# Optimization experiments

Measured on AMD Instinct MI355X. Metric: run time of the kernel, lower is better.

## Reference

```python
import jax, jax.numpy as jnp
from jax import lax
import numpy as np

GAMMA = 0.1
BIG = 1e8  # finite stand-in for +inf so grads/logsumexp stay clean

# solar radius in km; HUX propagates from 21.5 Rs (WSA inner boundary) to 1 AU (215 Rs)
RS_KM = 6.957e5
R0 = 21.5 * RS_KM
R1 = 215.0 * RS_KM
NR = 200  # radial steps (CFL ~ 0.5 for v~300 km/s, T=512)


def _hux(v_in, omega):
    """HUX-f upwind radial propagation. v_in: [B,T] km/s, omega: [B] rad/s."""
    B, T = v_in.shape
    dr = (R1 - R0) / NR
    dphi = 2.0 * jnp.pi / T  # one Carrington rotation over T samples
    om = omega[:, None]

    def step(v, _):
        dv = jnp.roll(v, -1, axis=1) - v  # periodic longitude
        v_new = v + (dr * om / (jnp.maximum(v, 1.0) * dphi)) * dv
        return v_new, None

    v_out, _ = lax.scan(step, v_in, None, length=NR)
    return v_out


def _soft_dtw(x, y, gamma):
    """Soft-DTW (Cuturi & Blondel). x,y: [B,T,1]. Returns [B]."""
    B, T, _ = x.shape
    # pairwise squared-euclidean cost  [B,T,T]
    D = jnp.sum((x[:, :, None, :] - y[:, None, :, :]) ** 2, axis=-1)
    i = jnp.arange(T)

    def softmin(a, b, c):
        return -gamma * jax.nn.logsumexp(-jnp.stack([a, b, c], 0) / gamma, axis=0)

    # anti-diagonal wavefront: r1[i] = R[i, p-1-i], r2[i] = R[i, p-2-i]
    def step(carry, p):
        r2, r1 = carry
        j = p - i
        valid = (j >= 0) & (j < T)
        d = D[:, i, jnp.clip(j, 0, T - 1)]          # [B,T] cost on diag p
        n_up = jnp.concatenate([jnp.full((B, 1), BIG, D.dtype), r1[:, :-1]], 1)   # R[i-1, p-i]
        n_left = r1                                                                # R[i, p-i-1]
        n_diag = jnp.concatenate([jnp.full((B, 1), BIG, D.dtype), r2[:, :-1]], 1)  # R[i-1, p-i-1]
        r_new = d + softmin(n_up, n_left, n_diag)
        r_new = jnp.where(valid[None, :], r_new, BIG)
        return (r1, r_new), None

    r0 = jnp.full((B, T), BIG, D.dtype).at[:, 0].set(D[:, 0, 0])  # diag p=0: R[0,0]=D[0,0]
    rm1 = jnp.full((B, T), BIG, D.dtype)
    (_, r_last), _ = lax.scan(step, (rm1, r0), jnp.arange(1, 2 * T - 1))
    return r_last[:, T - 1]  # R[T-1, T-1]


def _forward(pred_map, lat_idx, omega, omni_ts):
    B, _, H, W = pred_map.shape
    v_map = pred_map[:, 0]  # [B,H,W]
    T = lat_idx.shape[1]
    # v_in[b,t] = v_map[b, t, lat_idx[b,t]]
    v_in = jnp.take_along_axis(v_map[:, :T, :], lat_idx[:, :, None], axis=2)[..., 0]
    v_out = _hux(v_in, omega)

    v_out_scaled = (v_out - 200.0) / 1000.0
    omni_scaled = (omni_ts - 200.0) / 1000.0

    dtw_raw = _soft_dtw(omni_scaled[..., None], v_out_scaled[..., None], GAMMA)
    dtw_loss = jnp.abs(dtw_raw).mean()

    diff = v_out_scaled - omni_scaled
    rmse_loss = jnp.sqrt(jnp.sum(diff ** 2))
    mae_loss = jnp.sum(jnp.abs(diff))

    pc = v_out_scaled - v_out_scaled.mean(axis=1, keepdims=True)
    tc = omni_scaled - omni_scaled.mean(axis=1, keepdims=True)
    num = jnp.sum(pc * tc, axis=1)
    den = jnp.sqrt(jnp.sum(pc ** 2, axis=1)) * jnp.sqrt(jnp.sum(tc ** 2, axis=1))
    pcc_loss = 1.0 - (num / den).mean()

    return (v_out, mae_loss, pcc_loss, dtw_loss, rmse_loss)


def setup_inputs() -> dict:
    key = jax.random.key(0)
    k1, k2, k3, k4 = jax.random.split(key, 4)
    B, T, W = 32, 512, 128
    # realistic solar-wind speeds 300-700 km/s (keeps HUX stable and loss scaling sane)
    pred_map = 300.0 + 400.0 * jax.random.uniform(k1, (B, 1, T, W), dtype=jnp.float32)
    lat_idx = jax.random.randint(k2, (B, T), 0, W)
    omega = 2.7e-6 * (0.9 + 0.2 * jax.random.uniform(k3, (B,), dtype=jnp.float32))
    omni_ts = 300.0 + 400.0 * jax.random.uniform(k4, (B, T), dtype=jnp.float32)
    return {"pred_map": pred_map, "lat_idx": lat_idx, "omega": omega, "omni_ts": omni_ts}


def reference(pred_map, lat_idx, omega, omni_ts):
    return _forward(pred_map, lat_idx, omega, omni_ts)
```

## Files before the change

kernel.cpp:

```cpp
#include <hip/hip_runtime.h>
#include <math.h>

#define TT 512
#define NB 32
#define NRSTEP 200
#define KSC 14.4269504f

#define SCHR_SCALE (-KSC * 8388608.0f)
#define SCHR_OFF   1064986823.0f

typedef float float2v __attribute__((ext_vector_type(2)));

__device__ __forceinline__ float dpp_up1_f(float x) {
    return __int_as_float(__builtin_amdgcn_update_dpp(
        0, __float_as_int(x), 0x138, 0xf, 0xf, false));
}
__device__ __forceinline__ int dpp_up1_i(int x) {
    return __builtin_amdgcn_update_dpp(0, x, 0x138, 0xf, 0xf, false);
}
__device__ __forceinline__ float rdlane_f(float v, int lane) {
    return __int_as_float(__builtin_amdgcn_readlane(__float_as_int(v), lane));
}
__device__ __forceinline__ float exp2i(int e) {
    return __int_as_float((e + 127) << 23);
}

__global__ __launch_bounds__(64, 1) void fused_kernel(
    const float* __restrict__ pred_map,
    const int*   __restrict__ lat_idx,
    const float* __restrict__ omega,
    const float* __restrict__ omni,
    float*       __restrict__ out,
    float*       __restrict__ ws)
{
    const int b    = blockIdx.x;
    const int lane = threadIdx.x;
    const int t0   = lane * 8;
    const bool lane0 = (lane == 0);

    float v[8];
    const int*   li = lat_idx + b * TT + t0;
    const float* pm = pred_map + (size_t)b * TT * 128 + (size_t)t0 * 128;
    #pragma unroll
    for (int k = 0; k < 8; ++k) v[k] = pm[k * 128 + li[k]];

    const float c = (float)(673089.75 / (2.0 * M_PI / 512.0)) * omega[b];
    #pragma unroll 1
    for (int it = 0; it < NRSTEP; ++it) {
        float vn = __shfl(v[0], (lane + 1) & 63, 64);
        #pragma unroll
        for (int k = 0; k < 7; ++k) {
            float r = __builtin_amdgcn_rcpf(fmaxf(v[k], 1.0f));
            v[k] = v[k] + c * r * (v[k + 1] - v[k]);
        }
        float r7 = __builtin_amdgcn_rcpf(fmaxf(v[7], 1.0f));
        v[7] = v[7] + c * r7 * (vn - v[7]);
    }

    float4* o4 = (float4*)(out + b * TT + t0);
    o4[0] = make_float4(v[0], v[1], v[2], v[3]);
    o4[1] = make_float4(v[4], v[5], v[6], v[7]);

    float x[8], y8[8];
    const float* om = omni + b * TT + t0;
    float sx = 0.f, syy0 = 0.f;
    #pragma unroll
    for (int k = 0; k < 8; ++k) {
        x[k]  = (om[k] - 200.0f) * 1e-3f;
        y8[k] = (v[k] - 200.0f) * 1e-3f;
        sx += x[k];
        syy0 += y8[k];
    }
    #pragma unroll
    for (int m = 1; m < 64; m <<= 1) {
        sx   += __shfl_xor(sx, m, 64);
        syy0 += __shfl_xor(syy0, m, 64);
    }
    const float mx = sx * (1.0f / 512.0f);
    const float my = syy0 * (1.0f / 512.0f);

    float sab = 0.f, ssq = 0.f, snum = 0.f, sxx = 0.f, spp = 0.f;
    #pragma unroll
    for (int k = 0; k < 8; ++k) {
        float d = y8[k] - x[k];
        sab += fabsf(d);
        ssq += d * d;
        float pc = y8[k] - my;
        float tc = x[k] - mx;
        snum += pc * tc;
        sxx  += tc * tc;
        spp  += pc * pc;
    }
    #pragma unroll
    for (int m = 1; m < 64; m <<= 1) {
        sab  += __shfl_xor(sab,  m, 64);
        ssq  += __shfl_xor(ssq,  m, 64);
        snum += __shfl_xor(snum, m, 64);
        sxx  += __shfl_xor(sxx,  m, 64);
        spp  += __shfl_xor(spp,  m, 64);
    }
    const float corr = snum / (sqrtf(spp) * sqrtf(sxx));

    float2v x2[4];
    #pragma unroll
    for (int i = 0; i < 4; ++i) { x2[i].x = x[i]; x2[i].y = x[i + 4]; }

    float2v P[4];
    #pragma unroll
    for (int k = 0; k < 4; ++k) P[k] = (float2v){0.0f, 0.0f};
    int   E = 0;
    float c7w = 0.0f; int c7E = 0;
    float aT = 0.0f, aT2 = 0.0f;
    float pW = 0.0f;  int pE = 0;
    int   vj0 = -2 * lane;
    const float adoptW = lane0 ? 1.0f : 0.0f;

    float zA = lane0 ? y8[0] : 0.0f;
    float zB = 0.0f;

    #pragma unroll 1
    for (int blk = 0; blk < 80; ++blk) {
        const int us  = blk < 63 ? blk : 63;
        const int us1 = blk < 62 ? blk + 1 : 63;
        float f[8];
        f[0] = rdlane_f(y8[1], us);
        f[1] = rdlane_f(y8[2], us);
        f[2] = rdlane_f(y8[3], us);
        f[3] = rdlane_f(y8[4], us);
        f[4] = rdlane_f(y8[5], us);
        f[5] = rdlane_f(y8[6], us);
        f[6] = rdlane_f(y8[7], us);
        f[7] = rdlane_f(y8[0], us1);

        #pragma unroll
        for (int q = 0; q < 8; ++q) {
            float nW  = dpp_up1_f(c7w);
            int   nEc = dpp_up1_i(c7E);

            float2v z2; z2.x = zA; z2.y = zB;
            float2v fsv[4];
            #pragma unroll
            for (int i = 0; i < 4; ++i) {
                float2v t = x2[i] - z2;
                float2v h = (t * t) * (float2v){SCHR_SCALE, SCHR_SCALE}
                          + (float2v){SCHR_OFF, SCHR_OFF};
                fsv[i].x = __int_as_float((int)h.x);
                fsv[i].y = __int_as_float((int)h.y);
            }

            const bool adopt = (vj0 == 0);
            E = adopt ? nEc : E;
            float wuA = ldexpf(nW, E - nEc);
            float wdA = ldexpf(pW, E - pE);
            wdA = adopt ? adoptW : wdA;

            float2v uc, dgn;
            uc.x  = wuA; uc.y  = aT;
            dgn.x = wdA; dgn.y = aT2;
            #pragma unroll
            for (int k = 0; k < 4; ++k) {
                float2v wl = P[k];
                float2v a  = fsv[k] * (wl + dgn);
                float2v w  = fsv[k] * uc + a;
                dgn = wl; P[k] = w; uc = w;
            }
            aT2 = aT; aT = P[3].x;

            const bool pub = ((unsigned)(vj0 - 1) < 512u);
            c7w = pub ? P[3].y : c7w;
            c7E = pub ? E : c7E;
            pW = nW; pE = nEc;

            float zn = dpp_up1_f(zB);
            zB = zA;
            zA = lane0 ? f[q] : zn;
            ++vj0;
        }

        int ebits = (int)((__float_as_uint(P[3].y) >> 23) & 255u);
        int dsh = 127 - ebits;
        dsh = dsh > 126 ? 126 : (dsh < -126 ? -126 : dsh);
        float sf = exp2i(dsh);
        E += dsh;
        float2v sf2; sf2.x = sf; sf2.y = sf;
        #pragma unroll
        for (int k = 0; k < 4; ++k) P[k] = P[k] * sf2;
        aT *= sf; aT2 *= sf;
        c7w *= sf; c7E += dsh;
    }

    float dtwv = 0.0f;
    if (lane == 63) {
        float u = (float)c7E - __builtin_amdgcn_logf(c7w);
        dtwv = fabsf(u) * (1.0f / KSC);
    }

    int* cnt = (int*)(ws + 8);
    if (lane == 0) {
        atomicAdd(&ws[0], sab);
        atomicAdd(&ws[1], ssq);
        atomicAdd(&ws[2], corr);
    }
    if (lane == 63) atomicAdd(&ws[3], dtwv);
    __threadfence();
    if (lane == 0) {
        int prev = atomicAdd(cnt, 1);
        if (prev == NB - 1) {
            __threadfence();
            float mae  = atomicAdd(&ws[0], 0.0f);
            float sq   = atomicAdd(&ws[1], 0.0f);
            float pccs = atomicAdd(&ws[2], 0.0f);
            float dtws = atomicAdd(&ws[3], 0.0f);
            out[NB * TT + 0] = mae;
            out[NB * TT + 1] = 1.0f - pccs * (1.0f / 32.0f);
            out[NB * TT + 2] = dtws * (1.0f / 32.0f);
            out[NB * TT + 3] = sqrtf(sq);
        }
    }
}

extern "C" void kernel_launch(void* const* d_in, const int* in_sizes, int n_in,
                              void* d_out, int out_size, void* d_ws, size_t ws_size,
                              hipStream_t stream) {
    const float* pred_map = (const float*)d_in[0];
    const int*   lat_idx  = (const int*)d_in[1];
    const float* omega    = (const float*)d_in[2];
    const float* omni     = (const float*)d_in[3];
    float* out = (float*)d_out;
    float* ws  = (float*)d_ws;

    hipMemsetAsync(ws, 0, 64, stream);
    fused_kernel<<<NB, 64, 0, stream>>>(pred_map, lat_idx, omega, omni, out, ws);
}
```

Baseline: 153.6 us.

## Process two batches per wavefront to interleave independent dependency chains

Each 64-thread block now handles two batch elements instead of one, launching 16 blocks instead of 32. The HUX steps and the soft-DTW wavefront for both batches are interleaved, so the two independent serial chains can hide each other's instruction latency (DPP, readlane, FMA dependencies) within one wave. The cost is half as many blocks in flight, which leaves more CUs idle, and roughly double the register pressure per thread.

Measured after the change: 229.9 us. 1.5x slower.

```diff
diff --git a/kernel.cpp b/kernel.cpp
--- a/kernel.cpp
+++ b/kernel.cpp
@@ -3,6 +3,7 @@
 
 #define TT 512
 #define NB 32
+#define NBP 16
 #define NRSTEP 200
 #define KSC 14.4269504f
 
@@ -23,6 +24,71 @@
 }
 __device__ __forceinline__ float exp2i(int e) {
     return __int_as_float((e + 127) << 23);
+}
+
+struct DP {
+    float2v P[4];
+    int   E;
+    float c7w; int c7E;
+    float aT, aT2;
+    float pW;  int pE;
+    float zA, zB;
+};
+
+__device__ __forceinline__ void dp_substep(
+    DP& S, const float2v* x2, float fq, bool lane0, bool adopt, bool pub)
+{
+    float nW  = dpp_up1_f(S.c7w);
+    int   nEc = dpp_up1_i(S.c7E);
+
+    float2v z2; z2.x = S.zA; z2.y = S.zB;
+    float2v fsv[4];
+    #pragma unroll
+    for (int i = 0; i < 4; ++i) {
+        float2v t = x2[i] - z2;
+        float2v h = (t * t) * (float2v){SCHR_SCALE, SCHR_SCALE}
+                  + (float2v){SCHR_OFF, SCHR_OFF};
+        fsv[i].x = __int_as_float((int)h.x);
+        fsv[i].y = __int_as_float((int)h.y);
+    }
+
+    S.E = adopt ? nEc : S.E;
+    float wuA = ldexpf(nW, S.E - nEc);
+    float wdA = ldexpf(S.pW, S.E - S.pE);
+    wdA = adopt ? (lane0 ? 1.0f : 0.0f) : wdA;
+
+    float2v uc, dgn;
+    uc.x  = wuA; uc.y  = S.aT;
+    dgn.x = wdA; dgn.y = S.aT2;
+    #pragma unroll
+    for (int k = 0; k < 4; ++k) {
+        float2v wl = S.P[k];
+        float2v a  = fsv[k] * (wl + dgn);
+        float2v w  = fsv[k] * uc + a;
+        dgn = wl; S.P[k] = w; uc = w;
+    }
+    S.aT2 = S.aT; S.aT = S.P[3].x;
+
+    S.c7w = pub ? S.P[3].y : S.c7w;
+    S.c7E = pub ? S.E : S.c7E;
+    S.pW = nW; S.pE = nEc;
+
+    float zn = dpp_up1_f(S.zB);
+    S.zB = S.zA;
+    S.zA = lane0 ? fq : zn;
+}
+
+__device__ __forceinline__ void dp_renorm(DP& S) {
+    int ebits = (int)((__float_as_uint(S.P[3].y) >> 23) & 255u);
+    int dsh = 127 - ebits;
+    dsh = dsh > 126 ? 126 : (dsh < -126 ? -126 : dsh);
+    float sf = exp2i(dsh);
+    S.E += dsh;
+    float2v sf2; sf2.x = sf; sf2.y = sf;
+    #pragma unroll
+    for (int k = 0; k < 4; ++k) S.P[k] = S.P[k] * sf2;
+    S.aT *= sf; S.aT2 *= sf;
+    S.c7w *= sf; S.c7E += dsh;
 }
 
 __global__ __launch_bounds__(64, 1) void fused_kernel(
@@ -33,179 +99,154 @@
     float*       __restrict__ out,
     float*       __restrict__ ws)
 {
-    const int b    = blockIdx.x;
+    const int b0   = 2 * blockIdx.x;
+    const int b1   = b0 + 1;
     const int lane = threadIdx.x;
     const int t0   = lane * 8;
     const bool lane0 = (lane == 0);
 
-    float v[8];
-    const int*   li = lat_idx + b * TT + t0;
-    const float* pm = pred_map + (size_t)b * TT * 128 + (size_t)t0 * 128;
-    #pragma unroll
-    for (int k = 0; k < 8; ++k) v[k] = pm[k * 128 + li[k]];
-
-    const float c = (float)(673089.75 / (2.0 * M_PI / 512.0)) * omega[b];
+    float v0[8], v1[8];
+    const int*   li0 = lat_idx + b0 * TT + t0;
+    const int*   li1 = lat_idx + b1 * TT + t0;
+    const float* pm0 = pred_map + (size_t)b0 * TT * 128 + (size_t)t0 * 128;
+    const float* pm1 = pred_map + (size_t)b1 * TT * 128 + (size_t)t0 * 128;
+    #pragma unroll
+    for (int k = 0; k < 8; ++k) { v0[k] = pm0[k * 128 + li0[k]];
+                                  v1[k] = pm1[k * 128 + li1[k]]; }
+
+    const float c0 = (float)(673089.75 / (2.0 * M_PI / 512.0)) * omega[b0];
+    const float c1 = (float)(673089.75 / (2.0 * M_PI / 512.0)) * omega[b1];
     #pragma unroll 1
     for (int it = 0; it < NRSTEP; ++it) {
-        float vn = __shfl(v[0], (lane + 1) & 63, 64);
+        float vn0 = __shfl(v0[0], (lane + 1) & 63, 64);
+        float vn1 = __shfl(v1[0], (lane + 1) & 63, 64);
         #pragma unroll
         for (int k = 0; k < 7; ++k) {
-            float r = __builtin_amdgcn_rcpf(fmaxf(v[k], 1.0f));
-            v[k] = v[k] + c * r * (v[k + 1] - v[k]);
+            float r0 = __builtin_amdgcn_rcpf(fmaxf(v0[k], 1.0f));
+            float r1 = __builtin_amdgcn_rcpf(fmaxf(v1[k], 1.0f));
+            v0[k] = v0[k] + c0 * r0 * (v0[k + 1] - v0[k]);
+            v1[k] = v1[k] + c1 * r1 * (v1[k + 1] - v1[k]);
         }
-        float r7 = __builtin_amdgcn_rcpf(fmaxf(v[7], 1.0f));
-        v[7] = v[7] + c * r7 * (vn - v[7]);
-    }
-
-    float4* o4 = (float4*)(out + b * TT + t0);
-    o4[0] = make_float4(v[0], v[1], v[2], v[3]);
-    o4[1] = make_float4(v[4], v[5], v[6], v[7]);
-
-    float x[8], y8[8];
-    const float* om = omni + b * TT + t0;
-    float sx = 0.f, syy0 = 0.f;
+        float r70 = __builtin_amdgcn_rcpf(fmaxf(v0[7], 1.0f));
+        float r71 = __builtin_amdgcn_rcpf(fmaxf(v1[7], 1.0f));
+        v0[7] = v0[7] + c0 * r70 * (vn0 - v0[7]);
+        v1[7] = v1[7] + c1 * r71 * (vn1 - v1[7]);
+    }
+
+    float4* o40 = (float4*)(out + b0 * TT + t0);
+    float4* o41 = (float4*)(out + b1 * TT + t0);
+    o40[0] = make_float4(v0[0], v0[1], v0[2], v0[3]);
+    o40[1] = make_float4(v0[4], v0[5], v0[6], v0[7]);
+    o41[0] = make_float4(v1[0], v1[1], v1[2], v1[3]);
+    o41[1] = make_float4(v1[4], v1[5], v1[6], v1[7]);
+
+    float x0[8], y80[8], x1[8], y81[8];
+    const float* om0 = omni + b0 * TT + t0;
+    const float* om1 = omni + b1 * TT + t0;
+    float sx0 = 0.f, sy0 = 0.f, sx1 = 0.f, sy1 = 0.f;
     #pragma unroll
     for (int k = 0; k < 8; ++k) {
-        x[k]  = (om[k] - 200.0f) * 1e-3f;
-        y8[k] = (v[k] - 200.0f) * 1e-3f;
-        sx += x[k];
-        syy0 += y8[k];
+        x0[k]  = (om0[k] - 200.0f) * 1e-3f;
+        y80[k] = (v0[k] - 200.0f) * 1e-3f;
+        x1[k]  = (om1[k] - 200.0f) * 1e-3f;
+        y81[k] = (v1[k] - 200.0f) * 1e-3f;
+        sx0 += x0[k]; sy0 += y80[k];
+        sx1 += x1[k]; sy1 += y81[k];
     }
     #pragma unroll
     for (int m = 1; m < 64; m <<= 1) {
-        sx   += __shfl_xor(sx, m, 64);
-        syy0 += __shfl_xor(syy0, m, 64);
-    }
-    const float mx = sx * (1.0f / 512.0f);
-    const float my = syy0 * (1.0f / 512.0f);
-
-    float sab = 0.f, ssq = 0.f, snum = 0.f, sxx = 0.f, spp = 0.f;
+        sx0 += __shfl_xor(sx0, m, 64); sy0 += __shfl_xor(sy0, m, 64);
+        sx1 += __shfl_xor(sx1, m, 64); sy1 += __shfl_xor(sy1, m, 64);
+    }
+    const float mx0 = sx0 * (1.0f / 512.0f), my0 = sy0 * (1.0f / 512.0f);
+    const float mx1 = sx1 * (1.0f / 512.0f), my1 = sy1 * (1.0f / 512.0f);
+
+    float sab0 = 0.f, ssq0 = 0.f, snum0 = 0.f, sxx0 = 0.f, spp0 = 0.f;
+    float sab1 = 0.f, ssq1 = 0.f, snum1 = 0.f, sxx1 = 0.f, spp1 = 0.f;
     #pragma unroll
     for (int k = 0; k < 8; ++k) {
-        float d = y8[k] - x[k];
-        sab += fabsf(d);
-        ssq += d * d;
-        float pc = y8[k] - my;
-        float tc = x[k] - mx;
-        snum += pc * tc;
-        sxx  += tc * tc;
-        spp  += pc * pc;
+        float d0 = y80[k] - x0[k], d1 = y81[k] - x1[k];
+        sab0 += fabsf(d0); ssq0 += d0 * d0;
+        sab1 += fabsf(d1); ssq1 += d1 * d1;
+        float pc0 = y80[k] - my0, tc0 = x0[k] - mx0;
+        float pc1 = y81[k] - my1, tc1 = x1[k] - mx1;
+        snum0 += pc0 * tc0; sxx0 += tc0 * tc0; spp0 += pc0 * pc0;
+        snum1 += pc1 * tc1; sxx1 += tc1 * tc1; spp1 += pc1 * pc1;
     }
     #pragma unroll
     for (int m = 1; m < 64; m <<= 1) {
-        sab  += __shfl_xor(sab,  m, 64);
-        ssq  += __shfl_xor(ssq,  m, 64);
-        snum += __shfl_xor(snum, m, 64);
-        sxx  += __shfl_xor(sxx,  m, 64);
-        spp  += __shfl_xor(spp,  m, 64);
-    }
-    const float corr = snum / (sqrtf(spp) * sqrtf(sxx));
-
-    float2v x2[4];
-    #pragma unroll
-    for (int i = 0; i < 4; ++i) { x2[i].x = x[i]; x2[i].y = x[i + 4]; }
-
-    float2v P[4];
-    #pragma unroll
-    for (int k = 0; k < 4; ++k) P[k] = (float2v){0.0f, 0.0f};
-    int   E = 0;
-    float c7w = 0.0f; int c7E = 0;
-    float aT = 0.0f, aT2 = 0.0f;
-    float pW = 0.0f;  int pE = 0;
-    int   vj0 = -2 * lane;
-    const float adoptW = lane0 ? 1.0f : 0.0f;
-
-    float zA = lane0 ? y8[0] : 0.0f;
-    float zB = 0.0f;
+        sab0 += __shfl_xor(sab0, m, 64); ssq0 += __shfl_xor(ssq0, m, 64);
+        snum0 += __shfl_xor(snum0, m, 64); sxx0 += __shfl_xor(sxx0, m, 64);
+        spp0 += __shfl_xor(spp0, m, 64);
+        sab1 += __shfl_xor(sab1, m, 64); ssq1 += __shfl_xor(ssq1, m, 64);
+        snum1 += __shfl_xor(snum1, m, 64); sxx1 += __shfl_xor(sxx1, m, 64);
+        spp1 += __shfl_xor(spp1, m, 64);
+    }
+    const float corr0 = snum0 / (sqrtf(spp0) * sqrtf(sxx0));
+    const float corr1 = snum1 / (sqrtf(spp1) * sqrtf(sxx1));
+
+    float2v x20[4], x21[4];
+    #pragma unroll
+    for (int i = 0; i < 4; ++i) {
+        x20[i].x = x0[i]; x20[i].y = x0[i + 4];
+        x21[i].x = x1[i]; x21[i].y = x1[i + 4];
+    }
+
+    DP S0, S1;
+    #pragma unroll
+    for (int k = 0; k < 4; ++k) { S0.P[k] = (float2v){0.f, 0.f};
+                                  S1.P[k] = (float2v){0.f, 0.f}; }
+    S0.E = 0; S0.c7w = 0.f; S0.c7E = 0; S0.aT = 0.f; S0.aT2 = 0.f;
+    S0.pW = 0.f; S0.pE = 0; S0.zA = lane0 ? y80[0] : 0.f; S0.zB = 0.f;
+    S1.E = 0; S1.c7w = 0.f; S1.c7E = 0; S1.aT = 0.f; S1.aT2 = 0.f;
+    S1.pW = 0.f; S1.pE = 0; S1.zA = lane0 ? y81[0] : 0.f; S1.zB = 0.f;
+
+    int vj0 = -2 * lane;
 
     #pragma unroll 1
     for (int blk = 0; blk < 80; ++blk) {
         const int us  = blk < 63 ? blk : 63;
         const int us1 = blk < 62 ? blk + 1 : 63;
-        float f[8];
-        f[0] = rdlane_f(y8[1], us);
-        f[1] = rdlane_f(y8[2], us);
-        f[2] = rdlane_f(y8[3], us);
-        f[3] = rdlane_f(y8[4], us);
-        f[4] = rdlane_f(y8[5], us);
-        f[5] = rdlane_f(y8[6], us);
-        f[6] = rdlane_f(y8[7], us);
-        f[7] = rdlane_f(y8[0], us1);
+        float f0[8], f1[8];
+        f0[0] = rdlane_f(y80[1], us);  f1[0] = rdlane_f(y81[1], us);
+        f0[1] = rdlane_f(y80[2], us);  f1[1] = rdlane_f(y81[2], us);
+        f0[2] = rdlane_f(y80[3], us);  f1[2] = rdlane_f(y81[3], us);
+        f0[3] = rdlane_f(y80[4], us);  f1[3] = rdlane_f(y81[4], us);
+        f0[4] = rdlane_f(y80[5], us);  f1[4] = rdlane_f(y81[5], us);
+        f0[5] = rdlane_f(y80[6], us);  f1[5] = rdlane_f(y81[6], us);
+        f0[6] = rdlane_f(y80[7], us);  f1[6] = rdlane_f(y81[7], us);
+        f0[7] = rdlane_f(y80[0], us1); f1[7] = rdlane_f(y81[0], us1);
 
         #pragma unroll
         for (int q = 0; q < 8; ++q) {
-            float nW  = dpp_up1_f(c7w);
-            int   nEc = dpp_up1_i(c7E);
-
-            float2v z2; z2.x = zA; z2.y = zB;
-            float2v fsv[4];
-            #pragma unroll
-            for (int i = 0; i < 4; ++i) {
-                float2v t = x2[i] - z2;
-                float2v h = (t * t) * (float2v){SCHR_SCALE, SCHR_SCALE}
-                          + (float2v){SCHR_OFF, SCHR_OFF};
-                fsv[i].x = __int_as_float((int)h.x);
-                fsv[i].y = __int_as_float((int)h.y);
-            }
-
             const bool adopt = (vj0 == 0);
-            E = adopt ? nEc : E;
-            float wuA = ldexpf(nW, E - nEc);
-            float wdA = ldexpf(pW, E - pE);
-            wdA = adopt ? adoptW : wdA;
-
-            float2v uc, dgn;
-            uc.x  = wuA; uc.y  = aT;
-            dgn.x = wdA; dgn.y = aT2;
-            #pragma unroll
-            for (int k = 0; k < 4; ++k) {
-                float2v wl = P[k];
-                float2v a  = fsv[k] * (wl + dgn);
-                float2v w  = fsv[k] * uc + a;
-                dgn = wl; P[k] = w; uc = w;
-            }
-            aT2 = aT; aT = P[3].x;
-
-            const bool pub = ((unsigned)(vj0 - 1) < 512u);
-            c7w = pub ? P[3].y : c7w;
-            c7E = pub ? E : c7E;
-            pW = nW; pE = nEc;
-
-            float zn = dpp_up1_f(zB);
-            zB = zA;
-            zA = lane0 ? f[q] : zn;
+            const bool pub   = ((unsigned)(vj0 - 1) < 512u);
+            dp_substep(S0, x20, f0[q], lane0, adopt, pub);
+            dp_substep(S1, x21, f1[q], lane0, adopt, pub);
             ++vj0;
         }
-
-        int ebits = (int)((__float_as_uint(P[3].y) >> 23) & 255u);
-        int dsh = 127 - ebits;
-        dsh = dsh > 126 ? 126 : (dsh < -126 ? -126 : dsh);
-        float sf = exp2i(dsh);
-        E += dsh;
-        float2v sf2; sf2.x = sf; sf2.y = sf;
-        #pragma unroll
-        for (int k = 0; k < 4; ++k) P[k] = P[k] * sf2;
-        aT *= sf; aT2 *= sf;
-        c7w *= sf; c7E += dsh;
+        dp_renorm(S0);
+        dp_renorm(S1);
     }
 
     float dtwv = 0.0f;
     if (lane == 63) {
-        float u = (float)c7E - __builtin_amdgcn_logf(c7w);
-        dtwv = fabsf(u) * (1.0f / KSC);
+        float u0 = (float)S0.c7E - __builtin_amdgcn_logf(S0.c7w);
+        float u1 = (float)S1.c7E - __builtin_amdgcn_logf(S1.c7w);
+        dtwv = (fabsf(u0) + fabsf(u1)) * (1.0f / KSC);
     }
 
     int* cnt = (int*)(ws + 8);
     if (lane == 0) {
-        atomicAdd(&ws[0], sab);
-        atomicAdd(&ws[1], ssq);
-        atomicAdd(&ws[2], corr);
+        atomicAdd(&ws[0], sab0 + sab1);
+        atomicAdd(&ws[1], ssq0 + ssq1);
+        atomicAdd(&ws[2], corr0 + corr1);
     }
     if (lane == 63) atomicAdd(&ws[3], dtwv);
     __threadfence();
     if (lane == 0) {
         int prev = atomicAdd(cnt, 1);
-        if (prev == NB - 1) {
+        if (prev == NBP - 1) {
             __threadfence();
             float mae  = atomicAdd(&ws[0], 0.0f);
             float sq   = atomicAdd(&ws[1], 0.0f);
@@ -230,5 +271,5 @@
     float* ws  = (float*)d_ws;
 
     hipMemsetAsync(ws, 0, 64, stream);
-    fused_kernel<<<NB, 64, 0, stream>>>(pred_map, lat_idx, omega, omni, out, ws);
-}
+    fused_kernel<<<NBP, 64, 0, stream>>>(pred_map, lat_idx, omega, omni, out, ws);
+}
```
